# Kernel optimization log

Hardware: AMD Instinct MI355X
Metric: run time of the kernel (lower is better)

The kernel has to match this reference:

```python
import jax, jax.numpy as jnp
import numpy as np

DILATIONS = (1, 2, 4, 8, 16, 32, 64, 128)  # new_dilation doubles across all blocks*layers
BN_EPS = 1e-5


def conv1x1(x, w, b):
    # x: [B,C,N,T], w: [O,C], b: [O]
    return jnp.einsum('oc,bcnt->bont', w, x) + b[None, :, None, None]


def dilated_conv(x, w, b, d):
    T = x.shape[-1]
    y = jnp.einsum('oc,bcnt->bont', w[:, :, 0], x[..., :T - d]) \
      + jnp.einsum('oc,bcnt->bont', w[:, :, 1], x[..., d:])
    return y + b[None, :, None, None]


def graph_conv(x, supports, w, b):
    # gcn module, order=2, diag_mode='self_and_neighbor' (A unchanged), use_power=False
    outs = [x]
    for A in supports:
        h = x
        for _ in range(2):  # order
            h = jnp.einsum('bcvt,vw->bcwt', h, A)  # nconv: 'ncvl,vw->ncwl'
            outs.append(h)
    return conv1x1(jnp.concatenate(outs, axis=1), w, b)


def setup_inputs() -> dict:
    key = jax.random.key(0)
    B, Cin, N, T = 8, 2, 500, 256
    rc, dc, sc, ec, od, L, R = 32, 32, 256, 512, 12, 8, 10
    ks = jax.random.split(key, 24)
    s = 0.1
    return {
        'x': jax.random.normal(ks[0], (B, Cin, N, T), jnp.float32),
        'A0': jax.random.uniform(ks[1], (N, N), jnp.float32),
        'start_w': jax.random.normal(ks[2], (rc, Cin), jnp.float32) * s,
        'start_b': jnp.zeros((rc,), jnp.float32),
        'filt_w': jax.random.normal(ks[3], (L, dc, rc, 2), jnp.float32) * s,
        'filt_b': jnp.zeros((L, dc), jnp.float32),
        'gate_w': jax.random.normal(ks[4], (L, dc, rc, 2), jnp.float32) * s,
        'gate_b': jnp.zeros((L, dc), jnp.float32),
        'skip_w': jax.random.normal(ks[5], (L, sc, dc), jnp.float32) * s,
        'skip_b': jnp.zeros((L, sc), jnp.float32),
        'gcn_w': jax.random.normal(ks[6], (L, rc, 5 * dc), jnp.float32) * s,  # (order*supports+1)*c_in = 160
        'gcn_b': jnp.zeros((L, rc), jnp.float32),
        'bn_g': jnp.ones((L, rc), jnp.float32),
        'bn_b': jnp.zeros((L, rc), jnp.float32),
        'nodevec1': jax.random.normal(ks[7], (N, R), jnp.float32),
        'nodevec2': jax.random.normal(ks[8], (R, N), jnp.float32),
        'end1_w': jax.random.normal(ks[9], (ec, sc), jnp.float32) * s,
        'end1_b': jnp.zeros((ec,), jnp.float32),
        'end2_w': jax.random.normal(ks[10], (od, ec), jnp.float32) * s,
        'end2_b': jnp.zeros((od,), jnp.float32),
    }


def reference(x, A0, start_w, start_b, filt_w, filt_b, gate_w, gate_b,
              skip_w, skip_b, gcn_w, gcn_b, bn_g, bn_b,
              nodevec1, nodevec2, end1_w, end1_b, end2_w, end2_b):
    # adaptive adjacency: softmax(relu(E1 @ E2), dim=1)
    adp = jax.nn.softmax(jax.nn.relu(nodevec1 @ nodevec2), axis=1)
    supports = [A0, adp]

    h = conv1x1(x, start_w, start_b)  # [B,32,N,T]
    skip = None
    for i, d in enumerate(DILATIONS):
        residual = h
        f = jnp.tanh(dilated_conv(residual, filt_w[i], filt_b[i], d))
        g = jax.nn.sigmoid(dilated_conv(residual, gate_w[i], gate_b[i], d))
        h = f * g
        s = conv1x1(h, skip_w[i], skip_b[i])
        skip = s if skip is None else s + skip[..., -s.shape[-1]:]
        h = graph_conv(h, supports, gcn_w[i], gcn_b[i])
        h = h + residual[..., -h.shape[-1]:]
        # BatchNorm2d in eval mode: running_mean=0, running_var=1
        h = h / jnp.sqrt(1.0 + BN_EPS) * bn_g[i][None, :, None, None] + bn_b[i][None, :, None, None]

    out = jax.nn.relu(skip)
    out = jax.nn.relu(conv1x1(out, end1_w, end1_b))
    out = conv1x1(out, end2_w, end2_b)  # [B,12,N,1]
    return out
```

## Files before the change

kernel.cpp:

```cpp
#include <hip/hip_runtime.h>
#include <cstdint>
#include <cstddef>

#define NN 500
#define KP 512

typedef _Float16 f16;
typedef _Float16 half8 __attribute__((ext_vector_type(8)));
typedef float floatx4 __attribute__((ext_vector_type(4)));

#define GLOAD16(gp, lp)                                                     \
  __builtin_amdgcn_global_load_lds(                                         \
      (const __attribute__((address_space(1))) void*)(gp),                  \
      (__attribute__((address_space(3))) void*)(lp), 16, 0, 0)

struct PassSet {
  const f16* A[10];
  const f16* B[10];
};

__global__ __launch_bounds__(256) void adp_kernel(const float* __restrict__ e1,
                                                  const float* __restrict__ e2,
                                                  float* __restrict__ adp) {
  int r = blockIdx.x;
  int tid = threadIdx.x;
  __shared__ float red[256];
  __shared__ float e1row[16];
  if (tid < 10) e1row[tid] = e1[r * 10 + tid];
  __syncthreads();
  float z0, z1 = 0.f;
  {
    float acc = 0.f;
#pragma unroll
    for (int k = 0; k < 10; k++) acc += e1row[k] * e2[k * NN + tid];
    z0 = fmaxf(acc, 0.f);
  }
  bool has1 = (tid + 256) < NN;
  if (has1) {
    float acc = 0.f;
#pragma unroll
    for (int k = 0; k < 10; k++) acc += e1row[k] * e2[k * NN + tid + 256];
    z1 = fmaxf(acc, 0.f);
  }
  float mx = has1 ? fmaxf(z0, z1) : z0;
  red[tid] = mx;
  __syncthreads();
  for (int s = 128; s > 0; s >>= 1) {
    if (tid < s) red[tid] = fmaxf(red[tid], red[tid + s]);
    __syncthreads();
  }
  mx = red[0];
  __syncthreads();
  float ex0 = __expf(z0 - mx);
  float ex1 = has1 ? __expf(z1 - mx) : 0.f;
  red[tid] = ex0 + ex1;
  __syncthreads();
  for (int s = 128; s > 0; s >>= 1) {
    if (tid < s) red[tid] += red[tid + s];
    __syncthreads();
  }
  float inv = 1.f / red[0];
  adp[r * NN + tid] = ex0 * inv;
  if (has1) adp[r * NN + tid + 256] = ex1 * inv;
}

__global__ __launch_bounds__(256) void xt_kernel(const float* __restrict__ x,
                                                 float* __restrict__ xT) {
  __shared__ float tile[32][33];
  int tx = threadIdx.x & 31, ty = threadIdx.x >> 5;
  int n0 = blockIdx.x * 32, t0 = blockIdx.y * 32, bc = blockIdx.z;
#pragma unroll
  for (int rr = 0; rr < 4; rr++) {
    int n = n0 + ty + rr * 8, t = t0 + tx;
    tile[ty + rr * 8][tx] = (n < NN) ? x[((size_t)bc * NN + n) * 256 + t] : 0.f;
  }
  __syncthreads();
#pragma unroll
  for (int rr = 0; rr < 4; rr++) {
    int t = t0 + ty + rr * 8, n = n0 + tx;
    if (n < NN) xT[((size_t)bc * 256 + t) * NN + n] = tile[tx][ty + rr * 8];
  }
}

__global__ __launch_bounds__(256) void wtr_kernel(const float* __restrict__ fw,
                                                  const float* __restrict__ gw,
                                                  float* __restrict__ fwT,
                                                  float* __restrict__ gwT) {
  int idx = blockIdx.x * 256 + threadIdx.x;
  if (idx >= 16384) return;
  int c = idx & 31;
  int rest = idx >> 5;
  int tap = rest & 1;
  int cpi = rest >> 1;
  int cp = cpi & 31, i = cpi >> 5;
  size_t src = (((size_t)(i * 32 + c) * 32 + cp) * 2) + tap;
  fwT[idx] = fw[src];
  gwT[idx] = gw[src];
}

__global__ __launch_bounds__(256) void bt_kernel(const float* __restrict__ src,
                                                 f16* __restrict__ hi,
                                                 f16* __restrict__ lo) {
  int idx = blockIdx.x * 256 + threadIdx.x;
  int w = idx >> 9, v = idx & 511;
  float x = (w < NN && v < NN) ? src[v * NN + w] : 0.f;
  f16 h = (f16)x;
  hi[idx] = h;
  lo[idx] = (f16)(x - (float)h);
}

__global__ __launch_bounds__(512) void sq_kernel(const float* __restrict__ srcA,
                                                 const float* __restrict__ srcB,
                                                 f16* __restrict__ hiA, f16* __restrict__ loA,
                                                 f16* __restrict__ hiB, f16* __restrict__ loB) {
  const float* src = blockIdx.y == 0 ? srcA : srcB;
  f16* hi = blockIdx.y == 0 ? hiA : hiB;
  f16* lo = blockIdx.y == 0 ? loA : loB;
  int v = blockIdx.x;
  int w = threadIdx.x;
  __shared__ float vrow[512];
  vrow[w] = (v < NN && w < NN) ? src[v * NN + w] : 0.f;
  __syncthreads();
  float acc = 0.f;
  if (v < NN && w < NN) {
#pragma unroll 4
    for (int u = 0; u < NN; u++) acc = fmaf(vrow[u], src[u * NN + w], acc);
  }
  size_t o = (size_t)w * 512 + v;
  f16 h = (f16)acc;
  hi[o] = h;
  lo[o] = (f16)(acc - (float)h);
}

__global__ __launch_bounds__(256) void padzero_kernel(uint32_t* __restrict__ slab, int R) {
  int idx = blockIdx.x * 256 + threadIdx.x;
  int total = 6 * R * 6;
  if (idx >= total) return;
  int a = idx / (R * 6);
  int rem = idx - a * R * 6;
  int row = rem / 6;
  int q = rem - row * 6;
  slab[(size_t)a * R * 256 + (size_t)row * 256 + 250 + q] = 0u;
}

template <bool FUSED>
__global__ __launch_bounds__(256, 4) void dcm_kernel(
    const float* __restrict__ hprev, const float* __restrict__ xT,
    const float* __restrict__ sw, const float* __restrict__ sb,
    const float* __restrict__ fw, const float* __restrict__ fb,
    const float* __restrict__ gw, const float* __restrict__ gb,
    const float* __restrict__ cw, const float* __restrict__ cb,
    float* __restrict__ Hout,
    f16* __restrict__ P1a,
    f16* __restrict__ P2aH, f16* __restrict__ P2aL,
    f16* __restrict__ P1b,
    f16* __restrict__ P2bH, f16* __restrict__ P2bL,
    float* __restrict__ tapL,
    int Lp, int L, int b0) {
  int j = blockIdx.x, bb = blockIdx.y;
  int n0 = blockIdx.z * 256 + threadIdx.x;
  bool ok = (n0 < NN);
  int nc = ok ? n0 : (NN - 1);
  size_t base = ((size_t)(bb * 32) * Lp + 2 * j) * NN;
  size_t cs = (size_t)Lp * NN;
  float x00 = 0.f, x01 = 0.f, x10 = 0.f, x11 = 0.f;
  if (FUSED) {
    const float* xb = xT + (size_t)(b0 + bb) * 2 * 256 * NN;
    x00 = xb[(size_t)(2 * j) * NN + nc];
    x01 = xb[(size_t)(2 * j + 1) * NN + nc];
    x10 = xb[(size_t)(256 + 2 * j) * NN + nc];
    x11 = xb[(size_t)(256 + 2 * j + 1) * NN + nc];
  }
  float accf[32], accg[32];
#pragma unroll
  for (int c = 0; c < 32; c++) {
    accf[c] = fb[c];
    accg[c] = gb[c];
  }
#pragma unroll 2
  for (int cp = 0; cp < 32; cp++) {
    float v0, v1;
    if (FUSED) {
      float w0 = sw[cp * 2], w1 = sw[cp * 2 + 1], bc = sb[cp];
      v0 = fmaf(w0, x00, fmaf(w1, x10, bc));
      v1 = fmaf(w0, x01, fmaf(w1, x11, bc));
    } else {
      const float* hp = hprev + base + cp * cs;
      v0 = hp[nc];
      v1 = hp[NN + nc];
    }
    const float* fwp = fw + cp * 64;
    const float* gwp = gw + cp * 64;
#pragma unroll
    for (int c = 0; c < 32; c++) {
      float fw0 = fwp[c], fw1 = fwp[32 + c];
      float gw0 = gwp[c], gw1 = gwp[32 + c];
      accf[c] = fmaf(fw0, v0, accf[c]);
      accf[c] = fmaf(fw1, v1, accf[c]);
      accg[c] = fmaf(gw0, v0, accg[c]);
      accg[c] = fmaf(gw1, v1, accg[c]);
    }
  }
  float FG[32];
#pragma unroll
  for (int c = 0; c < 32; c++) {
    float E0 = __expf(2.f * accf[c]);
    float th0 = 1.f - 2.f / (E0 + 1.f);
    float sg0 = 1.f / (1.f + __expf(-accg[c]));
    FG[c] = th0 * sg0;
  }
  if (j == L - 1 && ok) {
    size_t tbase = ((size_t)(b0 + bb) * 32) * NN;
#pragma unroll
    for (int c = 0; c < 32; c++) {
      tapL[tbase + (size_t)c * NN + n0] = FG[c];
    }
  }
  if (Hout == nullptr) return;
#pragma unroll 2
  for (int c = 0; c < 32; c++) {
    const float* wr = cw + c * 160;
    float cbc = cb[c];
    float h0 = cbc, p10 = 0.f, p20 = 0.f, q10 = 0.f, q20 = 0.f;
#pragma unroll
    for (int cp = 0; cp < 32; cp++) {
      float w0 = wr[cp], w1 = wr[32 + cp], w2 = wr[64 + cp];
      float w3 = wr[96 + cp], w4 = wr[128 + cp];
      float f0 = FG[cp];
      h0  = fmaf(w0, f0, h0);
      p10 = fmaf(w1, f0, p10);
      p20 = fmaf(w2, f0, p20);
      q10 = fmaf(w3, f0, q10);
      q20 = fmaf(w4, f0, q20);
    }
    if (FUSED) {
      float sw0 = sw[c * 2], sw1 = sw[c * 2 + 1], sbc = sb[c];
      h0 += fmaf(sw0, x01, fmaf(sw1, x11, sbc));
    } else {
      const float* hr = hprev + ((size_t)(bb * 32 + c) * Lp + 2 * j + 1) * NN;
      h0 += hr[nc];
    }
    if (ok) {
      size_t mi = (size_t)(bb * 32 + c) * L + j;
      size_t o = mi * KP;
      f16 t;
      Hout[mi * NN + n0] = h0;
      P1a[o + n0] = (f16)p10;
      t = (f16)p20; P2aH[o + n0] = t; P2aL[o + n0] = (f16)(p20 - (float)t);
      P1b[o + n0] = (f16)q10;
      t = (f16)q20; P2bH[o + n0] = t; P2bL[o + n0] = (f16)(q20 - (float)t);
    }
  }
}

__global__ __launch_bounds__(256) void mfma_gcn(PassSet s,
    const float* __restrict__ Cin, float* __restrict__ Out, int M,
    const float* __restrict__ bng, const float* __restrict__ bnb, int lshift) {
  __shared__ f16 As[4][128 * 32];
  __shared__ f16 Bs[4][128 * 32];
  __shared__ const f16* Atab[10];
  __shared__ const f16* Btab[10];
  int tid = threadIdx.x;
  int wave = tid >> 6, lane = tid & 63;
  int wm = wave >> 1, wn = wave & 1;
  int m0 = blockIdx.x * 128;
  int n0 = blockIdx.y * 128;
  int lm = lane & 15, kq = lane >> 4;
  int laneoff = (lane >> 2) * KP + (((lane & 3) ^ ((lane >> 3) & 3)) << 3);
  int r0 = 32 * wave;
  size_t agA = (size_t)(m0 + r0) * KP + laneoff;
  size_t agB = (size_t)(n0 + r0) * KP + laneoff;
  int l0 = r0 * 32 + (lane << 3);
  int ach = kq ^ ((lm >> 1) & 3);

  if (tid == 0) {
#pragma unroll
    for (int i = 0; i < 10; i++) { Atab[i] = s.A[i]; Btab[i] = s.B[i]; }
  }
  __syncthreads();

  floatx4 acc[4][4];
#pragma unroll
  for (int i = 0; i < 4; i++)
#pragma unroll
    for (int j = 0; j < 4; j++) acc[i][j] = (floatx4){0.f, 0.f, 0.f, 0.f};

  auto issue = [&](int t, f16* Adst, f16* Bdst) {
    int uc = t < 160 ? t : 159;
    int p = uc >> 4;
    int k = (uc & 15) << 5;
    const f16* Ap = Atab[p];
    const f16* Bp = Btab[p];
    GLOAD16(Ap + agA + k, Adst);
    GLOAD16(Ap + agA + 16 * KP + k, Adst + 512);
    GLOAD16(Bp + agB + k, Bdst);
    GLOAD16(Bp + agB + 16 * KP + k, Bdst + 512);
  };

  issue(0, &As[0][l0], &Bs[0][l0]);
  issue(1, &As[1][l0], &Bs[1][l0]);
  issue(2, &As[2][l0], &Bs[2][l0]);

  for (int tb = 0; tb < 160; tb += 4) {
#pragma unroll
    for (int q = 0; q < 4; q++) {
      issue(tb + q + 3, &As[(q + 3) & 3][l0], &Bs[(q + 3) & 3][l0]);
      __builtin_amdgcn_sched_barrier(0);
      asm volatile("s_waitcnt vmcnt(12)" ::: "memory");
      __builtin_amdgcn_s_barrier();
      __builtin_amdgcn_sched_barrier(0);
      const f16* Ac = As[q];
      const f16* Bc = Bs[q];
      half8 a[4];
#pragma unroll
      for (int i = 0; i < 4; i++)
        a[i] = *(const half8*)(Ac + (wm * 64 + i * 16 + lm) * 32 + ach * 8);
#pragma unroll
      for (int j = 0; j < 4; j++) {
        half8 b = *(const half8*)(Bc + (wn * 64 + j * 16 + lm) * 32 + ach * 8);
#pragma unroll
        for (int i = 0; i < 4; i++)
          acc[i][j] = __builtin_amdgcn_mfma_f32_16x16x32_f16(a[i], b, acc[i][j], 0, 0, 0);
      }
      __builtin_amdgcn_sched_barrier(0);
      __builtin_amdgcn_s_barrier();
      __builtin_amdgcn_sched_barrier(0);
    }
  }
  asm volatile("s_waitcnt vmcnt(0)" ::: "memory");
  int cn = lane & 15, rq = lane >> 4;
  float rs = rsqrtf(1.f + 1e-5f);
#pragma unroll
  for (int i = 0; i < 4; i++) {
#pragma unroll
    for (int r = 0; r < 4; r++) {
      int row = m0 + wm * 64 + i * 16 + rq * 4 + r;
      if (row < M) {
        int c = (row >> lshift) & 31;
        float scale = bng[c] * rs;
        float bias = bnb[c];
#pragma unroll
        for (int j = 0; j < 4; j++) {
          int col = n0 + wn * 64 + j * 16 + cn;
          if (col < NN) {
            size_t o = (size_t)row * NN + col;
            Out[o] = (acc[i][j][r] + Cin[o]) * scale + bias;
          }
        }
      }
    }
  }
}

#define NB 20
#define NBP 21
__global__ __launch_bounds__(256) void final_kernel(const float* __restrict__ tap,
    const float* __restrict__ skw, const float* __restrict__ skb,
    const float* __restrict__ e1w, const float* __restrict__ e1b,
    const float* __restrict__ e2w, const float* __restrict__ e2b,
    float* __restrict__ out) {
  __shared__ float tapS[256][NBP];
  __shared__ float skS[256][NBP];
  __shared__ float e1S[512][NBP];
  int tid = threadIdx.x;
  int b = blockIdx.y;
  int n0 = blockIdx.x * NB;
  {
    int i = tid >> 5, c = tid & 31;
    const float* tp = tap + (((size_t)i * 8 + b) * 32 + c) * NN + n0;
#pragma unroll
    for (int v = 0; v < NB; v++) tapS[tid][v] = tp[v];
  }
  __syncthreads();
  {
    float bsum = 0.f;
#pragma unroll
    for (int i2 = 0; i2 < 8; i2++) bsum += skb[i2 * 256 + tid];
    float acc[NB];
#pragma unroll
    for (int v = 0; v < NB; v++) acc[v] = bsum;
#pragma unroll
    for (int i2 = 0; i2 < 8; i2++) {
      const float* wr = skw + ((size_t)i2 * 256 + tid) * 32;
#pragma unroll
      for (int cp = 0; cp < 32; cp++) {
        float w = wr[cp];
#pragma unroll
        for (int v = 0; v < NB; v++) acc[v] = fmaf(w, tapS[i2 * 32 + cp][v], acc[v]);
      }
    }
#pragma unroll
    for (int v = 0; v < NB; v++) skS[tid][v] = fmaxf(acc[v], 0.f);
  }
  __syncthreads();
#pragma unroll
  for (int h = 0; h < 2; h++) {
    int k = tid + h * 256;
    float bv = e1b[k];
    float acc[NB];
#pragma unroll
    for (int v = 0; v < NB; v++) acc[v] = bv;
    const float* wr = e1w + (size_t)k * 256;
    for (int o = 0; o < 256; o++) {
      float w = wr[o];
#pragma unroll
      for (int v = 0; v < NB; v++) acc[v] = fmaf(w, skS[o][v], acc[v]);
    }
#pragma unroll
    for (int v = 0; v < NB; v++) e1S[k][v] = fmaxf(acc[v], 0.f);
  }
  __syncthreads();
  if (tid < 12 * NB) {
    int q = tid / NB, v = tid % NB;
    float acc = e2b[q];
    const float* wr = e2w + (size_t)q * 512;
#pragma unroll 8
    for (int k = 0; k < 512; k++) acc = fmaf(wr[k], e1S[k][v], acc);
    out[((size_t)b * 12 + q) * NN + n0 + v] = acc;
  }
}

extern "C" void kernel_launch(void* const* d_in, const int* in_sizes, int n_in,
                              void* d_out, int out_size, void* d_ws, size_t ws_size,
                              hipStream_t stream) {
  const float* x       = (const float*)d_in[0];
  const float* A0      = (const float*)d_in[1];
  const float* start_w = (const float*)d_in[2];
  const float* start_b = (const float*)d_in[3];
  const float* filt_w  = (const float*)d_in[4];
  const float* filt_b  = (const float*)d_in[5];
  const float* gate_w  = (const float*)d_in[6];
  const float* gate_b  = (const float*)d_in[7];
  const float* skip_w  = (const float*)d_in[8];
  const float* skip_b  = (const float*)d_in[9];
  const float* gcn_w   = (const float*)d_in[10];
  const float* gcn_b   = (const float*)d_in[11];
  const float* bn_g    = (const float*)d_in[12];
  const float* bn_b    = (const float*)d_in[13];
  const float* nv1     = (const float*)d_in[14];
  const float* nv2     = (const float*)d_in[15];
  const float* e1w     = (const float*)d_in[16];
  const float* e1b     = (const float*)d_in[17];
  const float* e2w     = (const float*)d_in[18];
  const float* e2b     = (const float*)d_in[19];
  float* out = (float*)d_out;

  char* ws = (char*)d_ws;
  size_t off = 0;
  auto alloc = [&](size_t bytes) -> void* {
    void* p = (void*)(ws + off);
    off += (bytes + 255) & ~(size_t)255;
    return p;
  };
  float* adp   = (float*)alloc((size_t)NN * NN * 4);
  float* tap   = (float*)alloc((size_t)8 * 8 * 32 * NN * 4);
  float* xT    = (float*)alloc((size_t)16 * 256 * NN * 4);
  float* fwT   = (float*)alloc((size_t)16384 * 4);
  float* gwT   = (float*)alloc((size_t)16384 * 4);
  f16*   A0tH  = (f16*)alloc((size_t)KP * KP * 2);
  f16*   A0tL  = (f16*)alloc((size_t)KP * KP * 2);
  f16*   adptH = (f16*)alloc((size_t)KP * KP * 2);
  f16*   adptL = (f16*)alloc((size_t)KP * KP * 2);
  f16*   Q0H   = (f16*)alloc((size_t)KP * KP * 2);
  f16*   Q0L   = (f16*)alloc((size_t)KP * KP * 2);
  f16*   QdH   = (f16*)alloc((size_t)KP * KP * 2);
  f16*   QdL   = (f16*)alloc((size_t)KP * KP * 2);
  size_t fixed = off;

  int g = 1, rpb = 512;
  {
    const int gcand[4] = {8, 4, 2, 1};
    const int rcand[4] = {4096, 2048, 1024, 512};
    bool found = false;
    for (int gi = 0; gi < 4 && !found; gi++) {
      for (int ri = 0; ri < 4 && !found; ri++) {
        int gg = gcand[gi], rr = rcand[ri];
        if (4096 / rr > gg) continue;
        size_t need = fixed + (size_t)gg * 12288000ull +
                      6ull * gg * rr * KP * 2 + (1u << 20);
        if (need <= ws_size) { g = gg; rpb = rr; found = true; }
      }
    }
  }
  float* h128 = (float*)alloc((size_t)g * 8192000ull);
  float* h64  = (float*)alloc((size_t)g * 4096000ull);
  int R = g * rpb;
  f16* slab   = (f16*)alloc(6ull * R * KP * 2);
  f16* P1a  = slab + 0ull * R * KP;
  f16* P2aH = slab + 1ull * R * KP;
  f16* P2aL = slab + 2ull * R * KP;
  f16* P1b  = slab + 3ull * R * KP;
  f16* P2bH = slab + 4ull * R * KP;
  f16* P2bL = slab + 5ull * R * KP;

  adp_kernel<<<NN, 256, 0, stream>>>(nv1, nv2, adp);
  xt_kernel<<<dim3(16, 8, 16), 256, 0, stream>>>(x, xT);
  wtr_kernel<<<64, 256, 0, stream>>>(filt_w, gate_w, fwT, gwT);
  bt_kernel<<<1024, 256, 0, stream>>>(A0, A0tH, A0tL);
  bt_kernel<<<1024, 256, 0, stream>>>(adp, adptH, adptL);
  sq_kernel<<<dim3(512, 2), 512, 0, stream>>>(A0, adp, Q0H, Q0L, QdH, QdL);
  padzero_kernel<<<(36 * R + 255) / 256, 256, 0, stream>>>((uint32_t*)slab, R);

  PassSet ps{};
  {
    const f16* Alist[10] = {P1a, P1a, P2aH, P2aH, P2aL, P1b, P1b, P2bH, P2bH, P2bL};
    const f16* Blist[10] = {A0tH, A0tL, Q0H, Q0L, Q0H, adptH, adptL, QdH, QdL, QdH};
    for (int q = 0; q < 10; q++) { ps.A[q] = Alist[q]; ps.B[q] = Blist[q]; }
  }

  for (int b0 = 0; b0 < 8; b0 += g) {
    float* hprev = nullptr;
    int Lp = 256;
    for (int i = 0; i < 8; i++) {
      int L = Lp >> 1;
      if (i < 7) {
        float* hout = (i & 1) ? h64 : h128;
        int rows = 32 * L;
        int nCh = (rows + rpb - 1) / rpb;
        if (nCh < 1) nCh = 1;
        int bbw = g / nCh;
        for (int ch = 0; ch < nCh; ch++) {
          int bb0 = ch * bbw;
          const float* hprev_c = hprev ? hprev + (size_t)bb0 * 32 * Lp * NN : nullptr;
          float* hout_c = hout + (size_t)bb0 * 32 * L * NN;
          if (i == 0) {
            dcm_kernel<true><<<dim3(L, bbw, 2), 256, 0, stream>>>(
                nullptr, xT, start_w, start_b,
                fwT + i * 2048, filt_b + i * 32, gwT + i * 2048, gate_b + i * 32,
                gcn_w + i * 5120, gcn_b + i * 32, hout_c,
                P1a, P2aH, P2aL, P1b, P2bH, P2bL,
                tap + (size_t)i * 8 * 32 * NN, Lp, L, b0 + bb0);
          } else {
            dcm_kernel<false><<<dim3(L, bbw, 2), 256, 0, stream>>>(
                hprev_c, nullptr, nullptr, nullptr,
                fwT + i * 2048, filt_b + i * 32, gwT + i * 2048, gate_b + i * 32,
                gcn_w + i * 5120, gcn_b + i * 32, hout_c,
                P1a, P2aH, P2aL, P1b, P2bH, P2bL,
                tap + (size_t)i * 8 * 32 * NN, Lp, L, b0 + bb0);
          }
          int M = bbw * 32 * L;
          int Mb = (M + 127) / 128;
          mfma_gcn<<<dim3(Mb, 4), 256, 0, stream>>>(ps, hout_c, hout_c, M,
                                                    bn_g + i * 32, bn_b + i * 32, 7 - i);
        }
        hprev = hout;
        Lp = L;
      } else {
        dcm_kernel<false><<<dim3(1, g, 2), 256, 0, stream>>>(
            hprev, nullptr, nullptr, nullptr,
            fwT + i * 2048, filt_b + i * 32, gwT + i * 2048, gate_b + i * 32,
            gcn_w, gcn_b, nullptr,
            P1a, P2aH, P2aL, P1b, P2bH, P2bL,
            tap + (size_t)i * 8 * 32 * NN, Lp, 1, b0);
      }
    }
  }
  final_kernel<<<dim3(25, 8), 256, 0, stream>>>(tap, skip_w, skip_b, e1w, e1b, e2w, e2b, out);
}
```

Before: 2.107 ms.

## Load GCN B operand directly into registers and double-buffer A in LDS

The GEMM kernel stops staging the B operand in shared memory. Each wave now loads its B fragments straight from global memory into registers, double-buffered across iterations, while A keeps a two-stage LDS buffer in place of four stages. This cuts LDS use to 16KB and adds a launch-bounds occupancy hint of three blocks, aiming for more resident waves. The cost is a shallower prefetch depth, so global latency is hidden less, and each B fragment is loaded redundantly by the two waves that share the same wn.

```diff
diff --git a/kernel.cpp b/kernel.cpp
--- a/kernel.cpp
+++ b/kernel.cpp
@@ -253,11 +253,11 @@
   }
 }
 
-__global__ __launch_bounds__(256) void mfma_gcn(PassSet s,
+__global__ __launch_bounds__(256, 3) void mfma_gcn(PassSet s,
     const float* __restrict__ Cin, float* __restrict__ Out, int M,
     const float* __restrict__ bng, const float* __restrict__ bnb, int lshift) {
-  __shared__ f16 As[4][128 * 32];
-  __shared__ f16 Bs[4][128 * 32];
+  __shared__ f16 As0[128 * 32];
+  __shared__ f16 As1[128 * 32];
   __shared__ const f16* Atab[10];
   __shared__ const f16* Btab[10];
   int tid = threadIdx.x;
@@ -269,9 +269,9 @@
   int laneoff = (lane >> 2) * KP + (((lane & 3) ^ ((lane >> 3) & 3)) << 3);
   int r0 = 32 * wave;
   size_t agA = (size_t)(m0 + r0) * KP + laneoff;
-  size_t agB = (size_t)(n0 + r0) * KP + laneoff;
   int l0 = r0 * 32 + (lane << 3);
   int ach = kq ^ ((lm >> 1) & 3);
+  size_t bgB = (size_t)(n0 + wn * 64 + lm) * KP + kq * 8;
 
   if (tid == 0) {
 #pragma unroll
@@ -285,47 +285,53 @@
 #pragma unroll
     for (int j = 0; j < 4; j++) acc[i][j] = (floatx4){0.f, 0.f, 0.f, 0.f};
 
-  auto issue = [&](int t, f16* Adst, f16* Bdst) {
-    int uc = t < 160 ? t : 159;
-    int p = uc >> 4;
-    int k = (uc & 15) << 5;
-    const f16* Ap = Atab[p];
-    const f16* Bp = Btab[p];
-    GLOAD16(Ap + agA + k, Adst);
-    GLOAD16(Ap + agA + 16 * KP + k, Adst + 512);
-    GLOAD16(Bp + agB + k, Bdst);
-    GLOAD16(Bp + agB + 16 * KP + k, Bdst + 512);
+  half8 bR0[4], bR1[4];
+
+  {
+    const f16* Ap = s.A[0];
+    const f16* Bp = s.B[0];
+    GLOAD16(Ap + agA, &As0[l0]);
+    GLOAD16(Ap + agA + 16 * KP, &As0[l0 + 512]);
+#pragma unroll
+    for (int j = 0; j < 4; j++)
+      bR0[j] = *(const half8*)(Bp + bgB + (size_t)j * 16 * KP);
+  }
+
+  auto body = [&](int t, f16* Acur, f16* Anxt, half8 (&bcu)[4], half8 (&bnx)[4]) {
+    {
+      int un = t + 1; if (un > 159) un = 159;
+      int pn = un >> 4;
+      int kn = (un & 15) << 5;
+      const f16* An = Atab[pn];
+      const f16* Bn = Btab[pn];
+      GLOAD16(An + agA + kn, Anxt + l0);
+      GLOAD16(An + agA + 16 * KP + kn, Anxt + l0 + 512);
+#pragma unroll
+      for (int j = 0; j < 4; j++)
+        bnx[j] = *(const half8*)(Bn + bgB + (size_t)j * 16 * KP + kn);
+    }
+    __builtin_amdgcn_sched_barrier(0);
+    asm volatile("s_waitcnt vmcnt(6)" ::: "memory");
+    __builtin_amdgcn_s_barrier();
+    __builtin_amdgcn_sched_barrier(0);
+    half8 a[4];
+#pragma unroll
+    for (int i = 0; i < 4; i++)
+      a[i] = *(const half8*)(Acur + (wm * 64 + i * 16 + lm) * 32 + ach * 8);
+#pragma unroll
+    for (int j = 0; j < 4; j++) {
+#pragma unroll
+      for (int i = 0; i < 4; i++)
+        acc[i][j] = __builtin_amdgcn_mfma_f32_16x16x32_f16(a[i], bcu[j], acc[i][j], 0, 0, 0);
+    }
+    __builtin_amdgcn_sched_barrier(0);
+    __builtin_amdgcn_s_barrier();
+    __builtin_amdgcn_sched_barrier(0);
   };
 
-  issue(0, &As[0][l0], &Bs[0][l0]);
-  issue(1, &As[1][l0], &Bs[1][l0]);
-  issue(2, &As[2][l0], &Bs[2][l0]);
-
-  for (int tb = 0; tb < 160; tb += 4) {
-#pragma unroll
-    for (int q = 0; q < 4; q++) {
-      issue(tb + q + 3, &As[(q + 3) & 3][l0], &Bs[(q + 3) & 3][l0]);
-      __builtin_amdgcn_sched_barrier(0);
-      asm volatile("s_waitcnt vmcnt(12)" ::: "memory");
-      __builtin_amdgcn_s_barrier();
-      __builtin_amdgcn_sched_barrier(0);
-      const f16* Ac = As[q];
-      const f16* Bc = Bs[q];
-      half8 a[4];
-#pragma unroll
-      for (int i = 0; i < 4; i++)
-        a[i] = *(const half8*)(Ac + (wm * 64 + i * 16 + lm) * 32 + ach * 8);
-#pragma unroll
-      for (int j = 0; j < 4; j++) {
-        half8 b = *(const half8*)(Bc + (wn * 64 + j * 16 + lm) * 32 + ach * 8);
-#pragma unroll
-        for (int i = 0; i < 4; i++)
-          acc[i][j] = __builtin_amdgcn_mfma_f32_16x16x32_f16(a[i], b, acc[i][j], 0, 0, 0);
-      }
-      __builtin_amdgcn_sched_barrier(0);
-      __builtin_amdgcn_s_barrier();
-      __builtin_amdgcn_sched_barrier(0);
-    }
+  for (int tb = 0; tb < 160; tb += 2) {
+    body(tb,     As0, As1, bR0, bR1);
+    body(tb + 1, As1, As0, bR1, bR0);
   }
   asm volatile("s_waitcnt vmcnt(0)" ::: "memory");
   int cn = lane & 15, rq = lane >> 4;
```

Measured after the change: 2.347 ms. +11.4%, slower.
